# Optimization experiments

Hardware: AMD Instinct MI355X
Metric: run time of the kernel (lower is better)

## Reference

```python
import jax, jax.numpy as jnp
import numpy as np

N = 16384  # number of internal DAG nodes
L = 16384  # number of leaves


def setup_inputs() -> dict:
    key = jax.random.key(0)
    ks = jax.random.split(key, 12)
    idx = jnp.arange(N)
    # internal-child offsets and leaf ids
    off_l = jax.random.randint(ks[0], (N,), 1, N)
    off_r = jax.random.randint(ks[1], (N,), 1, N)
    leaf_l = jax.random.randint(ks[2], (N,), 0, L)
    leaf_r = jax.random.randint(ks[3], (N,), 0, L)
    is_int_l = (jax.random.uniform(ks[4], (N,)) < 0.5) & (idx < N - 1)
    is_int_r = (jax.random.uniform(ks[5], (N,)) < 0.5) & (idx < N - 1)
    # forward-pointing DAG: internal child index strictly greater than parent
    left = jnp.where(is_int_l, jnp.clip(idx + off_l, 0, N - 1), -(leaf_l + 1)).astype(jnp.int32)
    right = jnp.where(is_int_r, jnp.clip(idx + off_r, 0, N - 1), -(leaf_r + 1)).astype(jnp.int32)
    return {
        "thresholds": jax.random.normal(ks[6], (N,), dtype=jnp.float32),
        "rules": jax.random.randint(ks[7], (N,), 0, 16).astype(jnp.int32),
        "binary_ops": jax.random.randint(ks[8], (N,), 0, 8).astype(jnp.int32),
        "left": left,
        "right": right,
        "leaf_is_reroll": jax.random.uniform(ks[9], (L,)) < 0.5,
        "leaf_mask_left": jax.random.randint(ks[10], (L,), 0, 64).astype(jnp.int32),
        "leaf_mask_right": jax.random.randint(ks[11], (L,), 0, 64).astype(jnp.int32),
        "leaf_mask_op": jax.random.randint(jax.random.fold_in(key, 100), (L,), 0, 4).astype(jnp.int32),
        "leaf_score_cat": jax.random.randint(jax.random.fold_in(key, 101), (L,), 0, 16).astype(jnp.int32),
    }


def _active_mask(left, right, n_nodes):
    def step(reachable, _):
        active_left = jnp.where(reachable & (left >= 0), left, n_nodes)
        active_right = jnp.where(reachable & (right >= 0), right, n_nodes)
        new_reachable = jnp.zeros(n_nodes + 1, dtype=jnp.bool_)
        new_reachable = new_reachable.at[active_left].set(True)
        new_reachable = new_reachable.at[active_right].set(True)
        new_reachable = new_reachable.at[0].set(True)
        return new_reachable[:n_nodes] | reachable, None

    init = jnp.zeros(n_nodes, dtype=jnp.bool_).at[0].set(True)
    mask, _ = jax.lax.scan(step, init, None, length=n_nodes)
    return mask


def _subtree_leaf_flags(left, right, leaf_is_reroll, n):
    def is_leaf_score(child):
        leaf_id = -child - 1
        return (child < 0) & (~leaf_is_reroll[leaf_id])

    def is_leaf_reroll(child):
        leaf_id = -child - 1
        return (child < 0) & leaf_is_reroll[leaf_id]

    def step(carry, i):
        has_score, has_reroll = carry
        node = n - 1 - i  # postorder: children have larger indices
        l, r = left[node], right[node]

        def child_has_score(child):
            return is_leaf_score(child) | jnp.where(child >= 0, has_score[child], False)

        def child_has_reroll(child):
            return is_leaf_reroll(child) | jnp.where(child >= 0, has_reroll[child], False)

        has_score = has_score.at[node].set(child_has_score(l) | child_has_score(r))
        has_reroll = has_reroll.at[node].set(child_has_reroll(l) | child_has_reroll(r))
        return (has_score, has_reroll), None

    init = (jnp.zeros(n, dtype=jnp.bool_), jnp.zeros(n, dtype=jnp.bool_))
    (has_score, has_reroll), _ = jax.lax.scan(step, init, jnp.arange(n))
    return has_score, has_reroll


def reference(thresholds, rules, binary_ops, left, right, leaf_is_reroll,
              leaf_mask_left, leaf_mask_right, leaf_mask_op, leaf_score_cat):
    n = rules.shape[0]
    active_mask = _active_mask(left, right, n)
    has_score, has_reroll = _subtree_leaf_flags(left, right, leaf_is_reroll, n)
    active_node_count = jnp.sum(active_mask)
    return active_mask, has_score, has_reroll, active_node_count
```

## Files before the change

### kernel.cpp

```cpp
#include <hip/hip_runtime.h>

#define NN 16384
#define NT 1024
#define PER 16
#define KWIN 4

__global__ __launch_bounds__(NT) void dag_eval_kernel(
    const int* __restrict__ left,
    const int* __restrict__ right,
    const unsigned char* __restrict__ reroll_raw,
    int* __restrict__ out)
{
    __shared__ unsigned char reach[NN];
    __shared__ unsigned char state[NN + 16];
    __shared__ int flags[2];
    __shared__ int nzmask;
    __shared__ int cnt;

    const int tid = threadIdx.x;
    const int b0  = tid * PER;

    if (tid == 0) { nzmask = 0; cnt = 0; flags[0] = 0; flags[1] = 0; }
    if (tid < 16) state[NN + tid] = 4;

    int lch[PER], rch[PER];
    {
        const int4* l4 = (const int4*)left;
        const int4* r4 = (const int4*)right;
        #pragma unroll
        for (int j = 0; j < PER / 4; ++j) {
            int4 a = l4[(b0 >> 2) + j];
            int4 b = r4[(b0 >> 2) + j];
            lch[4*j+0] = a.x; lch[4*j+1] = a.y; lch[4*j+2] = a.z; lch[4*j+3] = a.w;
            rch[4*j+0] = b.x; rch[4*j+1] = b.y; rch[4*j+2] = b.z; rch[4*j+3] = b.w;
        }
    }

    {
        uint4 v = ((const uint4*)reroll_raw)[tid];
        unsigned int t = v.x | v.y | v.z | v.w;
        unsigned int m = 0;
        if (t & 0x000000FFu) m |= 1u;
        if (t & 0x0000FF00u) m |= 2u;
        if (t & 0x00FF0000u) m |= 4u;
        if (t & 0xFF000000u) m |= 8u;
        if (m) atomicOr(&nzmask, (int)m);
    }

    *(uint4*)&reach[b0] = make_uint4(0u, 0u, 0u, 0u);
    __syncthreads();

    const int mask   = nzmask;
    const int layout = ((mask & ~1) == 0) ? 0 : (((mask & 3) == 0) ? 1 : 2);
    const int*   ri = (const int*)reroll_raw;
    const float* rf = (const float*)reroll_raw;

    int sreg[PER];
    unsigned int todo = 0;
    #pragma unroll
    for (int k = 0; k < PER; ++k) {
        int s = 0;
        int l = lch[k], r = rch[k];
        if (l < 0) {
            int id = -l - 1;
            bool rr = (layout == 2) ? (reroll_raw[id] != 0)
                     : (layout == 1) ? (rf[id] != 0.0f)
                                     : (ri[id] != 0);
            s |= rr ? 2 : 1;
        }
        if (r < 0) {
            int id = -r - 1;
            bool rr = (layout == 2) ? (reroll_raw[id] != 0)
                     : (layout == 1) ? (rf[id] != 0.0f)
                                     : (ri[id] != 0);
            s |= rr ? 2 : 1;
        }
        if ((l < 0 && r < 0) || s == 3) s |= 4;
        else todo |= 1u << k;
        sreg[k] = s;
        state[b0 + k] = (unsigned char)s;
    }
    if (tid == 0) reach[0] = 1;
    __syncthreads();

    unsigned int pushed = 0, mm = 0;
    for (int w = 0; ; ++w) {
        bool ch = false;
        for (int it = 0; it < KWIN; ++it) {
            bool c2 = false;
            uint4 rv = *(const uint4*)&reach[b0];
            mm  =  ((rv.x * 0x01020408u) >> 24) & 0xFu;
            mm |= (((rv.y * 0x01020408u) >> 24) & 0xFu) << 4;
            mm |= (((rv.z * 0x01020408u) >> 24) & 0xFu) << 8;
            mm |= (((rv.w * 0x01020408u) >> 24) & 0xFu) << 12;
            unsigned int newp = mm & ~pushed;
            pushed |= newp;
            if (newp) c2 = true;
            while (newp) {
                int k = __builtin_ctz(newp);
                newp &= newp - 1u;
                int c = lch[k]; if (c >= 0) reach[c] = (unsigned char)1;
                c = rch[k];     if (c >= 0) reach[c] = (unsigned char)1;
            }
            if (todo) {
                int tl[PER], tr[PER];
                #pragma unroll
                for (int k = 0; k < PER; ++k) {
                    bool act = (todo >> k) & 1u;
                    int la = (act && lch[k] >= 0) ? lch[k] : NN;
                    int ra = (act && rch[k] >= 0) ? rch[k] : NN;
                    tl[k] = state[la];
                    tr[k] = state[ra];
                }
                #pragma unroll
                for (int k = 0; k < PER; ++k) {
                    if ((todo >> k) & 1u) {
                        int sl = tl[k], sr = tr[k];
                        int ns = sreg[k] | (sl & 3) | (sr & 3);
                        if (((sl & sr) & 4) || (ns & 3) == 3) {
                            ns |= 4;
                            todo &= ~(1u << k);
                            sreg[k] = ns;
                            state[b0 + k] = (unsigned char)ns;
                            c2 = true;
                        } else if (ns != sreg[k]) {
                            sreg[k] = ns;
                            state[b0 + k] = (unsigned char)ns;
                            c2 = true;
                        }
                    }
                }
            }
            ch |= c2;
            if (!c2) break;
        }
        int p = w & 1;
        if (ch) flags[p] = 1;
        __syncthreads();
        int f = flags[p];
        if (tid == 0) flags[p ^ 1] = 0;
        __syncthreads();
        if (!f) break;
    }

    int cc = __popc(mm);
    #pragma unroll
    for (int off = 32; off; off >>= 1) cc += __shfl_down(cc, off);
    if ((tid & 63) == 0) atomicAdd(&cnt, cc);

    int4* out4 = (int4*)out;
    #pragma unroll
    for (int j = 0; j < PER / 4; ++j) {
        int4 a, h, r;
        a.x = (mm >> (4*j+0)) & 1; a.y = (mm >> (4*j+1)) & 1;
        a.z = (mm >> (4*j+2)) & 1; a.w = (mm >> (4*j+3)) & 1;
        h.x =  sreg[4*j+0] & 1;       h.y =  sreg[4*j+1] & 1;
        h.z =  sreg[4*j+2] & 1;       h.w =  sreg[4*j+3] & 1;
        r.x = (sreg[4*j+0] >> 1) & 1; r.y = (sreg[4*j+1] >> 1) & 1;
        r.z = (sreg[4*j+2] >> 1) & 1; r.w = (sreg[4*j+3] >> 1) & 1;
        out4[(b0 >> 2) + j]              = a;
        out4[((NN + b0) >> 2) + j]       = h;
        out4[((2 * NN + b0) >> 2) + j]   = r;
    }
    __syncthreads();
    if (tid == 0) out[3 * NN] = cnt;
}

extern "C" void kernel_launch(void* const* d_in, const int* in_sizes, int n_in,
                              void* d_out, int out_size, void* d_ws, size_t ws_size,
                              hipStream_t stream)
{
    const int* left  = (const int*)d_in[3];
    const int* right = (const int*)d_in[4];
    const unsigned char* reroll = (const unsigned char*)d_in[5];
    int* out = (int*)d_out;
    dag_eval_kernel<<<1, NT, 0, stream>>>(left, right, reroll, out);
}
```

Before: 39.28 us.

## Halve threads, pack child indices as 16-bit, push grandchildren, sync every sweep

Switches to 512 threads with 32 nodes each and packs left/right child indices into 16-bit pairs, both in registers and in shared-memory tables. Reachability propagation now marks grandchildren directly from the shared child tables, which speeds frontier growth per sweep. The inner window now syncs the block after every sweep instead of looping locally, and sets the change flag eagerly. It also drops the separate gather array in the state update. This trades extra barriers and fewer threads for faster convergence and less register pressure.

```diff
diff --git a/kernel.cpp b/kernel.cpp
--- a/kernel.cpp
+++ b/kernel.cpp
@@ -1,8 +1,8 @@
 #include <hip/hip_runtime.h>
 
 #define NN 16384
-#define NT 1024
-#define PER 16
+#define NT 512
+#define PER 32
 #define KWIN 4
 
 __global__ __launch_bounds__(NT) void dag_eval_kernel(
@@ -11,8 +11,10 @@
     const unsigned char* __restrict__ reroll_raw,
     int* __restrict__ out)
 {
-    __shared__ unsigned char reach[NN];
-    __shared__ unsigned char state[NN + 16];
+    __shared__ __align__(16) unsigned char reach[NN];
+    __shared__ __align__(16) unsigned char state[NN + 16];
+    __shared__ __align__(16) unsigned int  l16w[NN / 2];
+    __shared__ __align__(16) unsigned int  r16w[NN / 2];
     __shared__ int flags[2];
     __shared__ int nzmask;
     __shared__ int cnt;
@@ -23,7 +25,7 @@
     if (tid == 0) { nzmask = 0; cnt = 0; flags[0] = 0; flags[1] = 0; }
     if (tid < 16) state[NN + tid] = 4;
 
-    int lch[PER], rch[PER];
+    unsigned int cpair[PER];
     {
         const int4* l4 = (const int4*)left;
         const int4* r4 = (const int4*)right;
@@ -31,14 +33,21 @@
         for (int j = 0; j < PER / 4; ++j) {
             int4 a = l4[(b0 >> 2) + j];
             int4 b = r4[(b0 >> 2) + j];
-            lch[4*j+0] = a.x; lch[4*j+1] = a.y; lch[4*j+2] = a.z; lch[4*j+3] = a.w;
-            rch[4*j+0] = b.x; rch[4*j+1] = b.y; rch[4*j+2] = b.z; rch[4*j+3] = b.w;
+            cpair[4*j+0] = (a.x & 0xFFFF) | (b.x << 16);
+            cpair[4*j+1] = (a.y & 0xFFFF) | (b.y << 16);
+            cpair[4*j+2] = (a.z & 0xFFFF) | (b.z << 16);
+            cpair[4*j+3] = (a.w & 0xFFFF) | (b.w << 16);
+            l16w[(b0 >> 1) + 2*j    ] = (a.x & 0xFFFF) | (a.y << 16);
+            l16w[(b0 >> 1) + 2*j + 1] = (a.z & 0xFFFF) | (a.w << 16);
+            r16w[(b0 >> 1) + 2*j    ] = (b.x & 0xFFFF) | (b.y << 16);
+            r16w[(b0 >> 1) + 2*j + 1] = (b.z & 0xFFFF) | (b.w << 16);
         }
     }
 
     {
-        uint4 v = ((const uint4*)reroll_raw)[tid];
-        unsigned int t = v.x | v.y | v.z | v.w;
+        const uint4* rv4 = (const uint4*)reroll_raw;
+        uint4 v0 = rv4[tid], v1 = rv4[tid + NT];
+        unsigned int t = v0.x | v0.y | v0.z | v0.w | v1.x | v1.y | v1.z | v1.w;
         unsigned int m = 0;
         if (t & 0x000000FFu) m |= 1u;
         if (t & 0x0000FF00u) m |= 2u;
@@ -47,7 +56,9 @@
         if (m) atomicOr(&nzmask, (int)m);
     }
 
-    *(uint4*)&reach[b0] = make_uint4(0u, 0u, 0u, 0u);
+    *(uint4*)&reach[b0]      = make_uint4(0u, 0u, 0u, 0u);
+    *(uint4*)&reach[b0 + 16] = make_uint4(0u, 0u, 0u, 0u);
+    if (tid == 0) reach[0] = 1;
     __syncthreads();
 
     const int mask   = nzmask;
@@ -59,84 +70,100 @@
     unsigned int todo = 0;
     #pragma unroll
     for (int k = 0; k < PER; ++k) {
+        int c0 = (int)(short)(cpair[k] & 0xFFFF);
+        int c1 = (int)(short)(cpair[k] >> 16);
         int s = 0;
-        int l = lch[k], r = rch[k];
-        if (l < 0) {
-            int id = -l - 1;
+        if (c0 < 0) {
+            int id = -c0 - 1;
             bool rr = (layout == 2) ? (reroll_raw[id] != 0)
                      : (layout == 1) ? (rf[id] != 0.0f)
                                      : (ri[id] != 0);
             s |= rr ? 2 : 1;
         }
-        if (r < 0) {
-            int id = -r - 1;
+        if (c1 < 0) {
+            int id = -c1 - 1;
             bool rr = (layout == 2) ? (reroll_raw[id] != 0)
                      : (layout == 1) ? (rf[id] != 0.0f)
                                      : (ri[id] != 0);
             s |= rr ? 2 : 1;
         }
-        if ((l < 0 && r < 0) || s == 3) s |= 4;
+        if ((c0 < 0 && c1 < 0) || s == 3) s |= 4;
         else todo |= 1u << k;
         sreg[k] = s;
         state[b0 + k] = (unsigned char)s;
     }
-    if (tid == 0) reach[0] = 1;
     __syncthreads();
 
     unsigned int pushed = 0, mm = 0;
     for (int w = 0; ; ++w) {
+        const int p = w & 1;
         bool ch = false;
         for (int it = 0; it < KWIN; ++it) {
-            bool c2 = false;
-            uint4 rv = *(const uint4*)&reach[b0];
-            mm  =  ((rv.x * 0x01020408u) >> 24) & 0xFu;
-            mm |= (((rv.y * 0x01020408u) >> 24) & 0xFu) << 4;
-            mm |= (((rv.z * 0x01020408u) >> 24) & 0xFu) << 8;
-            mm |= (((rv.w * 0x01020408u) >> 24) & 0xFu) << 12;
+            uint4 v0 = *(const uint4*)&reach[b0];
+            uint4 v1 = *(const uint4*)&reach[b0 + 16];
+            mm  =  ((v0.x * 0x01020408u) >> 24) & 0xFu;
+            mm |= (((v0.y * 0x01020408u) >> 24) & 0xFu) << 4;
+            mm |= (((v0.z * 0x01020408u) >> 24) & 0xFu) << 8;
+            mm |= (((v0.w * 0x01020408u) >> 24) & 0xFu) << 12;
+            mm |= (((v1.x * 0x01020408u) >> 24) & 0xFu) << 16;
+            mm |= (((v1.y * 0x01020408u) >> 24) & 0xFu) << 20;
+            mm |= (((v1.z * 0x01020408u) >> 24) & 0xFu) << 24;
+            mm |= (((v1.w * 0x01020408u) >> 24) & 0xFu) << 28;
             unsigned int newp = mm & ~pushed;
             pushed |= newp;
-            if (newp) c2 = true;
+            if (newp && !ch) { flags[p] = 1; ch = true; }
             while (newp) {
                 int k = __builtin_ctz(newp);
                 newp &= newp - 1u;
-                int c = lch[k]; if (c >= 0) reach[c] = (unsigned char)1;
-                c = rch[k];     if (c >= 0) reach[c] = (unsigned char)1;
+                int n = b0 + k;
+                unsigned int wl = l16w[n >> 1], wr = r16w[n >> 1];
+                int sh = (n & 1) * 16;
+                int c0 = (int)(short)((wl >> sh) & 0xFFFF);
+                int c1 = (int)(short)((wr >> sh) & 0xFFFF);
+                if (c0 > 0) {
+                    reach[c0] = (unsigned char)1;
+                    unsigned int gl = l16w[c0 >> 1], gr = r16w[c0 >> 1];
+                    int gs = (c0 & 1) * 16;
+                    int g0 = (int)(short)((gl >> gs) & 0xFFFF);
+                    int g1 = (int)(short)((gr >> gs) & 0xFFFF);
+                    if (g0 > 0) reach[g0] = (unsigned char)1;
+                    if (g1 > 0) reach[g1] = (unsigned char)1;
+                }
+                if (c1 > 0) {
+                    reach[c1] = (unsigned char)1;
+                    unsigned int gl = l16w[c1 >> 1], gr = r16w[c1 >> 1];
+                    int gs = (c1 & 1) * 16;
+                    int g0 = (int)(short)((gl >> gs) & 0xFFFF);
+                    int g1 = (int)(short)((gr >> gs) & 0xFFFF);
+                    if (g0 > 0) reach[g0] = (unsigned char)1;
+                    if (g1 > 0) reach[g1] = (unsigned char)1;
+                }
             }
             if (todo) {
-                int tl[PER], tr[PER];
+                unsigned int t = todo;
                 #pragma unroll
                 for (int k = 0; k < PER; ++k) {
-                    bool act = (todo >> k) & 1u;
-                    int la = (act && lch[k] >= 0) ? lch[k] : NN;
-                    int ra = (act && rch[k] >= 0) ? rch[k] : NN;
-                    tl[k] = state[la];
-                    tr[k] = state[ra];
-                }
-                #pragma unroll
-                for (int k = 0; k < PER; ++k) {
-                    if ((todo >> k) & 1u) {
-                        int sl = tl[k], sr = tr[k];
+                    if ((t >> k) & 1u) {
+                        int c0 = (int)(short)(cpair[k] & 0xFFFF);
+                        int c1 = (int)(short)(cpair[k] >> 16);
+                        int la = (c0 > 0) ? c0 : NN;
+                        int ra = (c1 > 0) ? c1 : NN;
+                        int sl = state[la];
+                        int sr = state[ra];
                         int ns = sreg[k] | (sl & 3) | (sr & 3);
-                        if (((sl & sr) & 4) || (ns & 3) == 3) {
-                            ns |= 4;
-                            todo &= ~(1u << k);
-                            sreg[k] = ns;
-                            state[b0 + k] = (unsigned char)ns;
-                            c2 = true;
-                        } else if (ns != sreg[k]) {
-                            sreg[k] = ns;
-                            state[b0 + k] = (unsigned char)ns;
-                            c2 = true;
+                        bool fin = ((sl & sr & 4) != 0) || ((ns & 3) == 3);
+                        int ns2 = fin ? (ns | 4) : ns;
+                        if (ns2 != sreg[k]) {
+                            sreg[k] = ns2;
+                            state[b0 + k] = (unsigned char)ns2;
+                            if (!ch) { flags[p] = 1; ch = true; }
                         }
+                        if (fin) todo &= ~(1u << k);
                     }
                 }
             }
-            ch |= c2;
-            if (!c2) break;
-        }
-        int p = w & 1;
-        if (ch) flags[p] = 1;
-        __syncthreads();
+            __syncthreads();
+        }
         int f = flags[p];
         if (tid == 0) flags[p ^ 1] = 0;
         __syncthreads();
@@ -158,9 +185,9 @@
         h.z =  sreg[4*j+2] & 1;       h.w =  sreg[4*j+3] & 1;
         r.x = (sreg[4*j+0] >> 1) & 1; r.y = (sreg[4*j+1] >> 1) & 1;
         r.z = (sreg[4*j+2] >> 1) & 1; r.w = (sreg[4*j+3] >> 1) & 1;
-        out4[(b0 >> 2) + j]              = a;
-        out4[((NN + b0) >> 2) + j]       = h;
-        out4[((2 * NN + b0) >> 2) + j]   = r;
+        out4[(b0 >> 2) + j]            = a;
+        out4[((NN + b0) >> 2) + j]     = h;
+        out4[((2 * NN + b0) >> 2) + j] = r;
     }
     __syncthreads();
     if (tid == 0) out[3 * NN] = cnt;
```

Result: slower. 45.62 us (+16.2%).

## Use one barrier per sweep with rotating flags and pack child pairs

Applied to the files above, without the earlier changes.

Removes the inner local-iteration window, so each sweep does one reach push and one state update, followed by a single barrier. A four-slot rotating convergence flag replaces the second barrier. Left and right child indices are packed as 16-bit halves of one register to cut register pressure, and the push loop becomes a fully unrolled predicated loop instead of a ctz-driven while loop. Without local iteration, more global sweeps may be needed. An iteration cap of 4096 is also added.

```diff
diff --git a/kernel.cpp b/kernel.cpp
--- a/kernel.cpp
+++ b/kernel.cpp
@@ -3,7 +3,6 @@
 #define NN 16384
 #define NT 1024
 #define PER 16
-#define KWIN 4
 
 __global__ __launch_bounds__(NT) void dag_eval_kernel(
     const int* __restrict__ left,
@@ -11,19 +10,20 @@
     const unsigned char* __restrict__ reroll_raw,
     int* __restrict__ out)
 {
-    __shared__ unsigned char reach[NN];
-    __shared__ unsigned char state[NN + 16];
-    __shared__ int flags[2];
+    __shared__ __align__(16) unsigned char reach[NN];
+    __shared__ __align__(16) unsigned char state[NN + 16];
+    __shared__ int flags[4];
     __shared__ int nzmask;
     __shared__ int cnt;
 
     const int tid = threadIdx.x;
     const int b0  = tid * PER;
 
-    if (tid == 0) { nzmask = 0; cnt = 0; flags[0] = 0; flags[1] = 0; }
+    if (tid < 4)  flags[tid] = 0;
+    if (tid == 0) { nzmask = 0; cnt = 0; }
     if (tid < 16) state[NN + tid] = 4;
 
-    int lch[PER], rch[PER];
+    unsigned int cpair[PER];
     {
         const int4* l4 = (const int4*)left;
         const int4* r4 = (const int4*)right;
@@ -31,8 +31,10 @@
         for (int j = 0; j < PER / 4; ++j) {
             int4 a = l4[(b0 >> 2) + j];
             int4 b = r4[(b0 >> 2) + j];
-            lch[4*j+0] = a.x; lch[4*j+1] = a.y; lch[4*j+2] = a.z; lch[4*j+3] = a.w;
-            rch[4*j+0] = b.x; rch[4*j+1] = b.y; rch[4*j+2] = b.z; rch[4*j+3] = b.w;
+            cpair[4*j+0] = (a.x & 0xFFFFu) | ((unsigned)b.x << 16);
+            cpair[4*j+1] = (a.y & 0xFFFFu) | ((unsigned)b.y << 16);
+            cpair[4*j+2] = (a.z & 0xFFFFu) | ((unsigned)b.z << 16);
+            cpair[4*j+3] = (a.w & 0xFFFFu) | ((unsigned)b.w << 16);
         }
     }
 
@@ -46,7 +48,6 @@
         if (t & 0xFF000000u) m |= 8u;
         if (m) atomicOr(&nzmask, (int)m);
     }
-
     *(uint4*)&reach[b0] = make_uint4(0u, 0u, 0u, 0u);
     __syncthreads();
 
@@ -59,23 +60,24 @@
     unsigned int todo = 0;
     #pragma unroll
     for (int k = 0; k < PER; ++k) {
+        int c0 = (int)(short)(cpair[k] & 0xFFFFu);
+        int c1 = (int)(short)(cpair[k] >> 16);
         int s = 0;
-        int l = lch[k], r = rch[k];
-        if (l < 0) {
-            int id = -l - 1;
+        if (c0 < 0) {
+            int id = -c0 - 1;
             bool rr = (layout == 2) ? (reroll_raw[id] != 0)
                      : (layout == 1) ? (rf[id] != 0.0f)
                                      : (ri[id] != 0);
             s |= rr ? 2 : 1;
         }
-        if (r < 0) {
-            int id = -r - 1;
+        if (c1 < 0) {
+            int id = -c1 - 1;
             bool rr = (layout == 2) ? (reroll_raw[id] != 0)
                      : (layout == 1) ? (rf[id] != 0.0f)
                                      : (ri[id] != 0);
             s |= rr ? 2 : 1;
         }
-        if ((l < 0 && r < 0) || s == 3) s |= 4;
+        if ((c0 < 0 && c1 < 0) || s == 3) s |= 4;
         else todo |= 1u << k;
         sreg[k] = s;
         state[b0 + k] = (unsigned char)s;
@@ -84,62 +86,61 @@
     __syncthreads();
 
     unsigned int pushed = 0, mm = 0;
-    for (int w = 0; ; ++w) {
+    for (int w = 0; w < 4096; ++w) {
         bool ch = false;
-        for (int it = 0; it < KWIN; ++it) {
-            bool c2 = false;
-            uint4 rv = *(const uint4*)&reach[b0];
-            mm  =  ((rv.x * 0x01020408u) >> 24) & 0xFu;
-            mm |= (((rv.y * 0x01020408u) >> 24) & 0xFu) << 4;
-            mm |= (((rv.z * 0x01020408u) >> 24) & 0xFu) << 8;
-            mm |= (((rv.w * 0x01020408u) >> 24) & 0xFu) << 12;
-            unsigned int newp = mm & ~pushed;
+
+        uint4 rv = *(const uint4*)&reach[b0];
+        mm  =  ((rv.x * 0x01020408u) >> 24) & 0xFu;
+        mm |= (((rv.y * 0x01020408u) >> 24) & 0xFu) << 4;
+        mm |= (((rv.z * 0x01020408u) >> 24) & 0xFu) << 8;
+        mm |= (((rv.w * 0x01020408u) >> 24) & 0xFu) << 12;
+        unsigned int newp = mm & ~pushed;
+        if (newp) {
             pushed |= newp;
-            if (newp) c2 = true;
-            while (newp) {
-                int k = __builtin_ctz(newp);
-                newp &= newp - 1u;
-                int c = lch[k]; if (c >= 0) reach[c] = (unsigned char)1;
-                c = rch[k];     if (c >= 0) reach[c] = (unsigned char)1;
+            ch = true;
+            #pragma unroll
+            for (int k = 0; k < PER; ++k) {
+                if ((newp >> k) & 1u) {
+                    int c0 = (int)(short)(cpair[k] & 0xFFFFu);
+                    int c1 = (int)(short)(cpair[k] >> 16);
+                    if (c0 > 0) reach[c0] = (unsigned char)1;
+                    if (c1 > 0) reach[c1] = (unsigned char)1;
+                }
             }
-            if (todo) {
-                int tl[PER], tr[PER];
-                #pragma unroll
-                for (int k = 0; k < PER; ++k) {
-                    bool act = (todo >> k) & 1u;
-                    int la = (act && lch[k] >= 0) ? lch[k] : NN;
-                    int ra = (act && rch[k] >= 0) ? rch[k] : NN;
-                    tl[k] = state[la];
-                    tr[k] = state[ra];
-                }
-                #pragma unroll
-                for (int k = 0; k < PER; ++k) {
-                    if ((todo >> k) & 1u) {
-                        int sl = tl[k], sr = tr[k];
-                        int ns = sreg[k] | (sl & 3) | (sr & 3);
-                        if (((sl & sr) & 4) || (ns & 3) == 3) {
-                            ns |= 4;
-                            todo &= ~(1u << k);
-                            sreg[k] = ns;
-                            state[b0 + k] = (unsigned char)ns;
-                            c2 = true;
-                        } else if (ns != sreg[k]) {
-                            sreg[k] = ns;
-                            state[b0 + k] = (unsigned char)ns;
-                            c2 = true;
-                        }
+        }
+
+        if (todo) {
+            int tl[PER], tr[PER];
+            #pragma unroll
+            for (int k = 0; k < PER; ++k) {
+                bool act = (todo >> k) & 1u;
+                int c0 = (int)(short)(cpair[k] & 0xFFFFu);
+                int c1 = (int)(short)(cpair[k] >> 16);
+                int la = (act && c0 > 0) ? c0 : NN;
+                int ra = (act && c1 > 0) ? c1 : NN;
+                tl[k] = state[la];
+                tr[k] = state[ra];
+            }
+            #pragma unroll
+            for (int k = 0; k < PER; ++k) {
+                if ((todo >> k) & 1u) {
+                    int sl = tl[k], sr = tr[k];
+                    int ns = sreg[k] | (sl & 3) | (sr & 3);
+                    bool fin = ((sl & sr & 4) != 0) || ((ns & 3) == 3);
+                    if (fin) { ns |= 4; todo &= ~(1u << k); }
+                    if (ns != sreg[k]) {
+                        sreg[k] = ns;
+                        state[b0 + k] = (unsigned char)ns;
+                        ch = true;
                     }
                 }
             }
-            ch |= c2;
-            if (!c2) break;
         }
-        int p = w & 1;
-        if (ch) flags[p] = 1;
+
+        if (ch) flags[w & 3] = 1;
         __syncthreads();
-        int f = flags[p];
-        if (tid == 0) flags[p ^ 1] = 0;
-        __syncthreads();
+        int f = flags[w & 3];
+        if (tid == 0) flags[(w + 2) & 3] = 0;
         if (!f) break;
     }
 
@@ -158,9 +159,9 @@
         h.z =  sreg[4*j+2] & 1;       h.w =  sreg[4*j+3] & 1;
         r.x = (sreg[4*j+0] >> 1) & 1; r.y = (sreg[4*j+1] >> 1) & 1;
         r.z = (sreg[4*j+2] >> 1) & 1; r.w = (sreg[4*j+3] >> 1) & 1;
-        out4[(b0 >> 2) + j]              = a;
-        out4[((NN + b0) >> 2) + j]       = h;
-        out4[((2 * NN + b0) >> 2) + j]   = r;
+        out4[(b0 >> 2) + j]            = a;
+        out4[((NN + b0) >> 2) + j]     = h;
+        out4[((2 * NN + b0) >> 2) + j] = r;
     }
     __syncthreads();
     if (tid == 0) out[3 * NN] = cnt;
```

Measured after the change: 32.84 us. -16.4%, faster.
